# Performance work log

Measured on AMD Instinct MI355X. Metric: run time of the kernel, lower is better.

Reference implementation:

```python
import jax, jax.numpy as jnp
import numpy as np

ALPHA = 0.01  # LeakyReLU negative slope
D_OUT = 128   # output_size; a1 is split at this index


def setup_inputs() -> dict:
    key = jax.random.key(0)
    k1, k2, k3, k4 = jax.random.split(key, 4)
    B, N, M, D_IN = 8, 2048, 2048, 256
    input_tensor1 = jax.random.normal(k1, (B, N, D_IN), dtype=jnp.float32)
    input_tensor2 = jax.random.normal(k2, (B, M, D_IN), dtype=jnp.float32)
    attention_mask2 = jnp.zeros((B, 1, M), dtype=jnp.float32)
    # Parameters (xavier-uniform-like scaled normals are fine for a numeric reference)
    W1 = jax.random.normal(k3, (D_IN, D_OUT), dtype=jnp.float32) * (1.414 * np.sqrt(2.0 / (D_IN + D_OUT)))
    a1 = jax.random.normal(k4, (2 * D_OUT, 1), dtype=jnp.float32) * (1.414 * np.sqrt(2.0 / (2 * D_OUT + 1)))
    return {"input_tensor1": input_tensor1, "input_tensor2": input_tensor2,
            "attention_mask2": attention_mask2, "W1": W1, "a1": a1}


def reference(input_tensor1, input_tensor2, attention_mask2, W1, a1):
    # Projections (dropout is identity in eval / p=0)
    Wh1 = jnp.einsum('bnd,de->bne', input_tensor1, W1)  # (B, N, E)
    Wh2 = jnp.einsum('bmd,de->bme', input_tensor2, W1)  # (B, M, E)
    # GAT-style additive score: broadcast outer-sum of two rank-1 projections
    att1 = jnp.einsum('bne,eo->bno', Wh1, a1[:D_OUT, :])   # (B, N, 1)
    att2 = jnp.einsum('bme,eo->bmo', Wh2, a1[D_OUT:, :])   # (B, M, 1)
    e = att1 + jnp.swapaxes(att2, 1, 2)                     # (B, N, M)
    e = jnp.where(e > 0, e, ALPHA * e)                      # LeakyReLU
    scores = e + attention_mask2                            # additive mask
    probs = jax.nn.softmax(scores, axis=-1)                 # (B, N, M)
    context = jnp.einsum('bnm,bme->bne', probs, Wh2)        # (B, N, E)
    return (context, probs)
```

## Files before the change

### kernel.cpp

```cpp
#include <hip/hip_runtime.h>

#define B 8
#define N 2048
#define M 2048
#define DIN 256
#define E 128
#define ALPHA 0.01f

typedef __attribute__((ext_vector_type(8))) short bf16x8;
typedef __attribute__((ext_vector_type(4))) float f32x4;

__device__ inline ushort f2bf(float x) {
  unsigned u = __float_as_uint(x);
  u = (u + 0x7FFFu + ((u >> 16) & 1u)) >> 16;
  return (ushort)u;
}

__device__ inline float leaky_mask(float a1r, float a2, float mk) {
  float s = a1r + a2;
  s = s > 0.f ? s : ALPHA * s;
  return s + mk;
}

__global__ __launch_bounds__(256) void prep_v_kernel(
    const float* __restrict__ W1, const float* __restrict__ a1,
    float* __restrict__ v1, float* __restrict__ v2) {
  int k = threadIdx.x;
  float s1 = 0.f, s2 = 0.f;
#pragma unroll 8
  for (int e = 0; e < E; ++e) {
    float w = W1[k * E + e];
    s1 += w * a1[e];
    s2 += w * a1[E + e];
  }
  v1[k] = s1;
  v2[k] = s2;
}

__global__ __launch_bounds__(256) void att_kernel(
    const float* __restrict__ in1, const float* __restrict__ in2,
    const float* __restrict__ v1, const float* __restrict__ v2,
    float* __restrict__ att1, float* __restrict__ att2) {
  int wave = blockIdx.x * 4 + (threadIdx.x >> 6);
  int lane = threadIdx.x & 63;
  const float* src;
  const float* v;
  float* dst;
  int row;
  if (wave < B * N) {
    src = in1; v = v1; dst = att1; row = wave;
  } else {
    src = in2; v = v2; dst = att2; row = wave - B * N;
  }
  float4 x = *(const float4*)(src + (size_t)row * DIN + lane * 4);
  float4 vv = *(const float4*)(v + lane * 4);
  float d = x.x * vv.x + x.y * vv.y + x.z * vv.z + x.w * vv.w;
#pragma unroll
  for (int off = 32; off; off >>= 1) d += __shfl_down(d, off, 64);
  if (lane == 0) dst[row] = d;
}

__global__ __launch_bounds__(256) void wh2_kernel(
    const float* __restrict__ in2, const float* __restrict__ W1,
    ushort* __restrict__ Wb) {
  __shared__ float a[32][DIN];
  int r0 = blockIdx.x * 32;
#pragma unroll
  for (int i = 0; i < 8; ++i) {
    int f = (threadIdx.x + i * 256) * 4;
    int r = f >> 8, k = f & 255;
    *(float4*)&a[r][k] = *(const float4*)(in2 + (size_t)(r0 + r) * DIN + k);
  }
  __syncthreads();
  int c  = (threadIdx.x & 31) * 4;
  int tr = (threadIdx.x >> 5) * 4;
  float acc[4][4] = {};
  for (int k = 0; k < DIN; ++k) {
    float4 b = *(const float4*)(W1 + k * E + c);
#pragma unroll
    for (int r = 0; r < 4; ++r) {
      float av = a[tr + r][k];
      acc[r][0] += av * b.x;
      acc[r][1] += av * b.y;
      acc[r][2] += av * b.z;
      acc[r][3] += av * b.w;
    }
  }
#pragma unroll
  for (int r = 0; r < 4; ++r) {
    int m = r0 + tr + r;
    size_t gbase = (size_t)(m >> 3) * 128 * 8 + (m & 7);
#pragma unroll
    for (int j = 0; j < 4; ++j)
      Wb[gbase + (size_t)(c + j) * 8] = f2bf(acc[r][j]);
  }
}

__global__ __launch_bounds__(256) void stats_kernel(
    const float* __restrict__ att1, const float* __restrict__ att2,
    const float* __restrict__ mask,
    float* __restrict__ rowmax, float* __restrict__ rowinv) {
  int row = blockIdx.x * 4 + (threadIdx.x >> 6);
  int lane = threadIdx.x & 63;
  int b = row >> 11;
  float a1r = att1[row];
  const float* a2 = att2 + b * M;
  const float* mk = mask + b * M;
  float mx = -1e30f;
#pragma unroll
  for (int i = 0; i < 8; ++i) {
    int m = (lane + i * 64) * 4;
    float4 av = *(const float4*)(a2 + m);
    float4 mv = *(const float4*)(mk + m);
    mx = fmaxf(mx, leaky_mask(a1r, av.x, mv.x));
    mx = fmaxf(mx, leaky_mask(a1r, av.y, mv.y));
    mx = fmaxf(mx, leaky_mask(a1r, av.z, mv.z));
    mx = fmaxf(mx, leaky_mask(a1r, av.w, mv.w));
  }
#pragma unroll
  for (int off = 32; off; off >>= 1) mx = fmaxf(mx, __shfl_xor(mx, off, 64));
  float sum = 0.f;
#pragma unroll
  for (int i = 0; i < 8; ++i) {
    int m = (lane + i * 64) * 4;
    float4 av = *(const float4*)(a2 + m);
    float4 mv = *(const float4*)(mk + m);
    sum += __expf(leaky_mask(a1r, av.x, mv.x) - mx);
    sum += __expf(leaky_mask(a1r, av.y, mv.y) - mx);
    sum += __expf(leaky_mask(a1r, av.z, mv.z) - mx);
    sum += __expf(leaky_mask(a1r, av.w, mv.w) - mx);
  }
#pragma unroll
  for (int off = 32; off; off >>= 1) sum += __shfl_xor(sum, off, 64);
  if (lane == 0) {
    rowmax[row] = mx;
    rowinv[row] = 1.f / sum;
  }
}

__global__ __launch_bounds__(256) void fused_kernel(
    const float* __restrict__ att1, const float* __restrict__ att2,
    const float* __restrict__ mask, const float* __restrict__ rowmax,
    const float* __restrict__ rowinv, const ushort* __restrict__ Wb,
    float* __restrict__ probs, float* __restrict__ ctx) {
  __shared__ float att2s[M];
  __shared__ float masks[M];
  __shared__ ushort ldsB[2 * 8 * 128 * 8];

  int rt = blockIdx.x & 63;
  int b  = blockIdx.x >> 6;
  int row0 = b * N + rt * 32;
  int t = threadIdx.x;
  int lane = t & 63;
  int w = t >> 6;
  int quad = lane >> 4;
  int l16 = lane & 15;
  int m0w = (w & 1) * 16;
  int h   = w >> 1;

#pragma unroll
  for (int i = 0; i < 2; ++i) {
    int idx = (t + i * 256) * 4;
    *(float4*)&att2s[idx] = *(const float4*)(att2 + b * M + idx);
    *(float4*)&masks[idx] = *(const float4*)(mask + b * M + idx);
  }

  int myrow = row0 + m0w + l16;
  float a1v  = att1[myrow];
  float rmxL = rowmax[myrow];
  float rinL = rowinv[myrow];
  float* prow = probs + (size_t)myrow * M;

  f32x4 acc[8] = {};

  for (int k0 = 0; k0 < M; k0 += 128) {
    {
      const char* g =
          (const char*)(Wb + ((size_t)b * 256 + (k0 >> 3)) * 1024);
      char* l = (char*)ldsB;
      int base = w * 1024 + lane * 16;
#pragma unroll
      for (int i = 0; i < 8; ++i) {
        int off = base + i * 4096;
        __builtin_amdgcn_global_load_lds(
            (const __attribute__((address_space(1))) void*)(g + off),
            (__attribute__((address_space(3))) void*)(l + off), 16, 0, 0);
      }
    }
    __syncthreads();
    int kc = k0 + h * 64;
#pragma unroll
    for (int ks = 0; ks < 64; ks += 32) {
      int kb = kc + ks + quad * 8;
      float4 a0 = *(const float4*)&att2s[kb];
      float4 a1q = *(const float4*)&att2s[kb + 4];
      float4 k0v = *(const float4*)&masks[kb];
      float4 k1v = *(const float4*)&masks[kb + 4];
      float p[8];
      p[0] = __expf(leaky_mask(a1v, a0.x, k0v.x) - rmxL) * rinL;
      p[1] = __expf(leaky_mask(a1v, a0.y, k0v.y) - rmxL) * rinL;
      p[2] = __expf(leaky_mask(a1v, a0.z, k0v.z) - rmxL) * rinL;
      p[3] = __expf(leaky_mask(a1v, a0.w, k0v.w) - rmxL) * rinL;
      p[4] = __expf(leaky_mask(a1v, a1q.x, k1v.x) - rmxL) * rinL;
      p[5] = __expf(leaky_mask(a1v, a1q.y, k1v.y) - rmxL) * rinL;
      p[6] = __expf(leaky_mask(a1v, a1q.z, k1v.z) - rmxL) * rinL;
      p[7] = __expf(leaky_mask(a1v, a1q.w, k1v.w) - rmxL) * rinL;
      bf16x8 af;
#pragma unroll
      for (int j = 0; j < 8; ++j) af[j] = (short)f2bf(p[j]);
      *(float4*)(prow + kb)     = make_float4(p[0], p[1], p[2], p[3]);
      *(float4*)(prow + kb + 4) = make_float4(p[4], p[5], p[6], p[7]);
      int gl = h * 8 + (ks >> 3) + quad;
#pragma unroll
      for (int cf = 0; cf < 8; ++cf) {
        int n = cf * 16 + l16;
        bf16x8 bfb = *(const bf16x8*)&ldsB[((size_t)gl * 128 + n) * 8];
        acc[cf] =
            __builtin_amdgcn_mfma_f32_16x16x32_bf16(af, bfb, acc[cf], 0, 0, 0);
      }
    }
    __syncthreads();
  }

  float* red = (float*)ldsB;
  if (h == 1) {
    int base = ((w & 1) * 64 + lane) * 36;
#pragma unroll
    for (int cf = 0; cf < 8; ++cf)
      *(f32x4*)&red[base + cf * 4] = acc[cf];
  }
  __syncthreads();
  if (h == 0) {
    int base = ((w & 1) * 64 + lane) * 36;
#pragma unroll
    for (int cf = 0; cf < 8; ++cf) {
      f32x4 o = *(const f32x4*)&red[base + cf * 4];
      int nn = cf * 16 + l16;
#pragma unroll
      for (int reg = 0; reg < 4; ++reg) {
        int rr = row0 + m0w + quad * 4 + reg;
        ctx[(size_t)rr * E + nn] = acc[cf][reg] + o[reg];
      }
    }
  }
}

extern "C" void kernel_launch(void* const* d_in, const int* in_sizes, int n_in,
                              void* d_out, int out_size, void* d_ws,
                              size_t ws_size, hipStream_t stream) {
  (void)in_sizes; (void)n_in; (void)out_size; (void)ws_size;
  const float* in1  = (const float*)d_in[0];
  const float* in2  = (const float*)d_in[1];
  const float* mask = (const float*)d_in[2];
  const float* W1   = (const float*)d_in[3];
  const float* a1   = (const float*)d_in[4];

  float* ws     = (float*)d_ws;
  float* v1     = ws;
  float* v2     = v1 + DIN;
  float* att1   = v2 + DIN;
  float* att2   = att1 + B * N;
  float* rowmax = att2 + B * M;
  float* rowinv = rowmax + B * N;
  ushort* Wb    = (ushort*)(rowinv + B * N);

  float* ctx   = (float*)d_out;
  float* probs = ctx + (size_t)B * N * E;

  hipLaunchKernelGGL(prep_v_kernel, dim3(1), dim3(256), 0, stream, W1, a1, v1, v2);
  hipLaunchKernelGGL(att_kernel, dim3((B * N + B * M) / 4), dim3(256), 0, stream,
                     in1, in2, v1, v2, att1, att2);
  hipLaunchKernelGGL(wh2_kernel, dim3(B * M / 32), dim3(256), 0, stream,
                     in2, W1, Wb);
  hipLaunchKernelGGL(stats_kernel, dim3(B * N / 4), dim3(256), 0, stream,
                     att1, att2, mask, rowmax, rowinv);
  hipLaunchKernelGGL(fused_kernel, dim3(B * N / 32), dim3(256), 0, stream,
                     att1, att2, mask, rowmax, rowinv, Wb, probs, ctx);
}
```

Baseline: 228.5 us.

## Split K across four waves per 16-row tile, read Wh2 from global directly

The fused softmax-times-V kernel now gives each block 16 rows instead of 32. Its four waves split the M reduction into 512-wide chunks and combine partial accumulators with a two-stage LDS reduction. The LDS staging of Wh2 through global_load_lds, and the barriers inside the loop, are removed; B fragments are loaded straight from global memory (L2/L1). This doubles the grid, lowers LDS use for higher occupancy (launch bounds 256,4), and drops per-iteration syncs. The cost is that each block re-reads all of Wh2 for half as many rows, doubling global/L2 traffic for B.

```diff
diff --git a/kernel.cpp b/kernel.cpp
--- a/kernel.cpp
+++ b/kernel.cpp
@@ -138,25 +138,24 @@
   }
 }
 
-__global__ __launch_bounds__(256) void fused_kernel(
+__global__ __launch_bounds__(256, 4) void fused_kernel(
     const float* __restrict__ att1, const float* __restrict__ att2,
     const float* __restrict__ mask, const float* __restrict__ rowmax,
     const float* __restrict__ rowinv, const ushort* __restrict__ Wb,
     float* __restrict__ probs, float* __restrict__ ctx) {
-  __shared__ float att2s[M];
-  __shared__ float masks[M];
-  __shared__ ushort ldsB[2 * 8 * 128 * 8];
-
-  int rt = blockIdx.x & 63;
-  int b  = blockIdx.x >> 6;
-  int row0 = b * N + rt * 32;
+  __shared__ float smem[2 * 64 * 36];
+  float* att2s = smem;
+  float* masks = smem + 2048;
+
+  int blk = blockIdx.x;
+  int b   = blk >> 7;
+  int rt  = blk & 127;
+  int row0 = b * N + rt * 16;
   int t = threadIdx.x;
   int lane = t & 63;
   int w = t >> 6;
   int quad = lane >> 4;
   int l16 = lane & 15;
-  int m0w = (w & 1) * 16;
-  int h   = w >> 1;
 
 #pragma unroll
   for (int i = 0; i < 2; ++i) {
@@ -164,81 +163,80 @@
     *(float4*)&att2s[idx] = *(const float4*)(att2 + b * M + idx);
     *(float4*)&masks[idx] = *(const float4*)(mask + b * M + idx);
   }
-
-  int myrow = row0 + m0w + l16;
+  __syncthreads();
+
+  int myrow = row0 + l16;
   float a1v  = att1[myrow];
   float rmxL = rowmax[myrow];
   float rinL = rowinv[myrow];
   float* prow = probs + (size_t)myrow * M;
+  const ushort* wbb = Wb + (size_t)b * M * E;
 
   f32x4 acc[8] = {};
-
-  for (int k0 = 0; k0 < M; k0 += 128) {
-    {
-      const char* g =
-          (const char*)(Wb + ((size_t)b * 256 + (k0 >> 3)) * 1024);
-      char* l = (char*)ldsB;
-      int base = w * 1024 + lane * 16;
-#pragma unroll
-      for (int i = 0; i < 8; ++i) {
-        int off = base + i * 4096;
-        __builtin_amdgcn_global_load_lds(
-            (const __attribute__((address_space(1))) void*)(g + off),
-            (__attribute__((address_space(3))) void*)(l + off), 16, 0, 0);
-      }
-    }
-    __syncthreads();
-    int kc = k0 + h * 64;
-#pragma unroll
-    for (int ks = 0; ks < 64; ks += 32) {
-      int kb = kc + ks + quad * 8;
-      float4 a0 = *(const float4*)&att2s[kb];
-      float4 a1q = *(const float4*)&att2s[kb + 4];
-      float4 k0v = *(const float4*)&masks[kb];
-      float4 k1v = *(const float4*)&masks[kb + 4];
-      float p[8];
-      p[0] = __expf(leaky_mask(a1v, a0.x, k0v.x) - rmxL) * rinL;
-      p[1] = __expf(leaky_mask(a1v, a0.y, k0v.y) - rmxL) * rinL;
-      p[2] = __expf(leaky_mask(a1v, a0.z, k0v.z) - rmxL) * rinL;
-      p[3] = __expf(leaky_mask(a1v, a0.w, k0v.w) - rmxL) * rinL;
-      p[4] = __expf(leaky_mask(a1v, a1q.x, k1v.x) - rmxL) * rinL;
-      p[5] = __expf(leaky_mask(a1v, a1q.y, k1v.y) - rmxL) * rinL;
-      p[6] = __expf(leaky_mask(a1v, a1q.z, k1v.z) - rmxL) * rinL;
-      p[7] = __expf(leaky_mask(a1v, a1q.w, k1v.w) - rmxL) * rinL;
-      bf16x8 af;
-#pragma unroll
-      for (int j = 0; j < 8; ++j) af[j] = (short)f2bf(p[j]);
-      *(float4*)(prow + kb)     = make_float4(p[0], p[1], p[2], p[3]);
-      *(float4*)(prow + kb + 4) = make_float4(p[4], p[5], p[6], p[7]);
-      int gl = h * 8 + (ks >> 3) + quad;
-#pragma unroll
-      for (int cf = 0; cf < 8; ++cf) {
-        int n = cf * 16 + l16;
-        bf16x8 bfb = *(const bf16x8*)&ldsB[((size_t)gl * 128 + n) * 8];
-        acc[cf] =
-            __builtin_amdgcn_mfma_f32_16x16x32_bf16(af, bfb, acc[cf], 0, 0, 0);
-      }
-    }
-    __syncthreads();
-  }
-
-  float* red = (float*)ldsB;
-  if (h == 1) {
-    int base = ((w & 1) * 64 + lane) * 36;
-#pragma unroll
-    for (int cf = 0; cf < 8; ++cf)
-      *(f32x4*)&red[base + cf * 4] = acc[cf];
-  }
-  __syncthreads();
-  if (h == 0) {
-    int base = ((w & 1) * 64 + lane) * 36;
+  int kbase = w * 512;
+
+  for (int ks = 0; ks < 512; ks += 32) {
+    int kb = kbase + ks + quad * 8;
+    float4 a0  = *(const float4*)&att2s[kb];
+    float4 a1q = *(const float4*)&att2s[kb + 4];
+    float4 m0  = *(const float4*)&masks[kb];
+    float4 m1  = *(const float4*)&masks[kb + 4];
+    float p[8];
+    p[0] = __expf(leaky_mask(a1v, a0.x, m0.x) - rmxL) * rinL;
+    p[1] = __expf(leaky_mask(a1v, a0.y, m0.y) - rmxL) * rinL;
+    p[2] = __expf(leaky_mask(a1v, a0.z, m0.z) - rmxL) * rinL;
+    p[3] = __expf(leaky_mask(a1v, a0.w, m0.w) - rmxL) * rinL;
+    p[4] = __expf(leaky_mask(a1v, a1q.x, m1.x) - rmxL) * rinL;
+    p[5] = __expf(leaky_mask(a1v, a1q.y, m1.y) - rmxL) * rinL;
+    p[6] = __expf(leaky_mask(a1v, a1q.z, m1.z) - rmxL) * rinL;
+    p[7] = __expf(leaky_mask(a1v, a1q.w, m1.w) - rmxL) * rinL;
+    bf16x8 af;
+#pragma unroll
+    for (int j = 0; j < 8; ++j) af[j] = (short)f2bf(p[j]);
+    *(float4*)(prow + kb)     = make_float4(p[0], p[1], p[2], p[3]);
+    *(float4*)(prow + kb + 4) = make_float4(p[4], p[5], p[6], p[7]);
+    const ushort* bptr = wbb + (size_t)(kb >> 3) * 1024;
+#pragma unroll
+    for (int cf = 0; cf < 8; ++cf) {
+      bf16x8 bfb = *(const bf16x8*)(bptr + (cf * 16 + l16) * 8);
+      acc[cf] =
+          __builtin_amdgcn_mfma_f32_16x16x32_bf16(af, bfb, acc[cf], 0, 0, 0);
+    }
+  }
+
+  __syncthreads();
+  float* red = smem;
+  if (w >= 2) {
+    int base = (w - 2) * 64 * 36 + lane * 36;
+#pragma unroll
+    for (int cf = 0; cf < 8; ++cf) *(f32x4*)&red[base + cf * 4] = acc[cf];
+  }
+  __syncthreads();
+  if (w < 2) {
+    int base = w * 64 * 36 + lane * 36;
+#pragma unroll
+    for (int cf = 0; cf < 8; ++cf) {
+      f32x4 o = *(const f32x4*)&red[base + cf * 4];
+      acc[cf][0] += o[0]; acc[cf][1] += o[1];
+      acc[cf][2] += o[2]; acc[cf][3] += o[3];
+    }
+  }
+  __syncthreads();
+  if (w == 1) {
+    int base = lane * 36;
+#pragma unroll
+    for (int cf = 0; cf < 8; ++cf) *(f32x4*)&red[base + cf * 4] = acc[cf];
+  }
+  __syncthreads();
+  if (w == 0) {
+    int base = lane * 36;
 #pragma unroll
     for (int cf = 0; cf < 8; ++cf) {
       f32x4 o = *(const f32x4*)&red[base + cf * 4];
       int nn = cf * 16 + l16;
 #pragma unroll
       for (int reg = 0; reg < 4; ++reg) {
-        int rr = row0 + m0w + quad * 4 + reg;
+        int rr = row0 + quad * 4 + reg;
         ctx[(size_t)rr * E + nn] = acc[cf][reg] + o[reg];
       }
     }
@@ -274,6 +272,6 @@
                      in2, W1, Wb);
   hipLaunchKernelGGL(stats_kernel, dim3(B * N / 4), dim3(256), 0, stream,
                      att1, att2, mask, rowmax, rowinv);
-  hipLaunchKernelGGL(fused_kernel, dim3(B * N / 32), dim3(256), 0, stream,
+  hipLaunchKernelGGL(fused_kernel, dim3(B * N / 16), dim3(256), 0, stream,
                      att1, att2, mask, rowmax, rowinv, Wb, probs, ctx);
 }
```

Result: slower. 246.3 us (+7.8%).
